# Optimization experiments

Measured on AMD Instinct MI355X. Metric: run time of the kernel, lower is better.

Reference implementation:

```python
import jax, jax.numpy as jnp
import numpy as np

BS = 320        # batch_size (per-view)
D = 128         # projection feature dim
SIGMA = 0.07    # rbf gamma = 1/sigma
C_BOX = 1.0     # box constraint on alpha
REG = 0.1       # diagonal regularizer


def setup_inputs() -> dict:
    key = jax.random.key(0)
    z = jax.random.normal(key, (2 * BS, D), dtype=jnp.float32)
    return {"z": z}


def reference(z):
    bs = z.shape[0] // 2
    nn_ = bs - 1
    dtype = z.dtype

    # L2-normalize features
    z = z / jnp.linalg.norm(z, axis=1, keepdims=True)

    gamma = 1.0 / float(SIGMA)
    K = jnp.exp(-gamma * (2.0 - 2.0 * (z[:bs] @ z.T)))        # (bs, 2bs)

    # ---- QP assembly (no-grad in original) ----
    KK = jax.lax.stop_gradient(K[:, :bs])                      # (bs, bs)
    eye = jnp.eye(bs, dtype=dtype)
    KK_d0 = KK * (1.0 - eye)
    # Delta[t,i,j] = 1 + reg*eye[i,j] + KK[i,j] - KK_d0[t,i] - KK_d0[t,j]
    Delta = (1.0 + REG * eye + KK)[None, :, :] \
            - KK_d0[:, None, :] - KK_d0[:, :, None]            # (bs, bs, bs)

    # For each t, drop row t and column t -> (bs, nn, nn)
    t_idx = jnp.arange(bs)
    j = jnp.arange(nn_)
    idx = j[None, :] + (j[None, :] >= t_idx[:, None]).astype(j.dtype)  # (bs, nn)
    DD = Delta[t_idx[:, None, None], idx[:, :, None], idx[:, None, :]]

    # Batched linear solve: DD alpha = 2*1
    rhs = 2.0 * jnp.ones((bs, nn_, 1), dtype=dtype)
    alpha_y = jnp.linalg.solve(DD, rhs)[..., 0]                # (bs, nn)
    alpha_y = jax.lax.stop_gradient(
        jnp.clip(jax.nn.relu(alpha_y), 0.0, C_BOX))
    alpha_x = alpha_y.sum(1)                                   # (bs,)

    # ---- loss terms (grad flows through K here) ----
    Ks = K[:, bs:]                                             # (bs, bs)
    # Kn = Ks^T with diagonal removed row-wise, then transposed -> (nn, bs)
    Kn = Ks.T[t_idx[:, None], idx].T

    pos_terms = jnp.diagonal(Ks)                               # (Ks * pos_mask).sum(1)
    pos_loss = (alpha_x * pos_terms).mean()
    neg_loss = (alpha_y.T * Kn).sum() / bs
    loss = neg_loss - pos_loss

    num_zero = (alpha_y == 0).sum().astype(dtype) / alpha_y.size
    sparsity = (alpha_y == C_BOX).sum().astype(dtype) / \
               ((alpha_y > 0).sum().astype(dtype) + 1e-10)

    return (loss, pos_terms.mean(), Kn.mean(), sparsity, num_zero, 0.0)
```

## Files before the change

### kernel.cpp

```cpp
#include <hip/hip_runtime.h>
#include <math.h>

#define BSZ 320
#define N2  640
#define DIM 128
#define GAM (1.0/0.07)

__device__ __forceinline__ double wave_red(double v) {
    #pragma unroll
    for (int off = 32; off > 0; off >>= 1) v += __shfl_down(v, off, 64);
    return v;
}

__launch_bounds__(640)
__global__ void k_gram(const float* __restrict__ z, double* __restrict__ E,
                       double* __restrict__ KnT, double* __restrict__ rE,
                       double* __restrict__ ssq, int* __restrict__ counter) {
    const int j  = threadIdx.x;
    const int i0 = blockIdx.x * 2;
    __shared__ float  zc[N2][36];
    __shared__ double sE[2][10], sQ[2][10];
    __shared__ double szi[2];

    if (blockIdx.x == 0 && j == 0) *counter = 0;

    double rr = 0.0;
    float  cr0 = 0.f, cr1 = 0.f;

    for (int kc = 0; kc < 4; kc++) {
        const int k0 = kc * 32;
        __syncthreads();
        #pragma unroll
        for (int it = 0; it < 8; it++) {
            int f = it * 640 + j;
            int row = f >> 3, c4 = f & 7;
            *(float4*)&zc[row][c4 * 4] = *(const float4*)(z + row * DIM + k0 + c4 * 4);
        }
        __syncthreads();
        #pragma unroll
        for (int k4 = 0; k4 < 8; k4++) {
            float4 b  = *(const float4*)&zc[j][k4 * 4];
            float4 a0 = *(const float4*)&zc[i0][k4 * 4];
            float4 a1 = *(const float4*)&zc[i0 + 1][k4 * 4];
            cr0 = fmaf(a0.x, b.x, cr0); cr1 = fmaf(a1.x, b.x, cr1);
            rr = fma((double)b.x, (double)b.x, rr);
            cr0 = fmaf(a0.y, b.y, cr0); cr1 = fmaf(a1.y, b.y, cr1);
            rr = fma((double)b.y, (double)b.y, rr);
            cr0 = fmaf(a0.z, b.z, cr0); cr1 = fmaf(a1.z, b.z, cr1);
            rr = fma((double)b.z, (double)b.z, rr);
            cr0 = fmaf(a0.w, b.w, cr0); cr1 = fmaf(a1.w, b.w, cr1);
            rr = fma((double)b.w, (double)b.w, rr);
        }
    }

    double sinv = 1.0 / sqrt(rr);
    if (j == i0)     szi[0] = sinv;
    if (j == i0 + 1) szi[1] = sinv;
    __syncthreads();
    double c0 = (double)cr0 * szi[0] * sinv;
    double c1 = (double)cr1 * szi[1] * sinv;
    double v0 = exp(-GAM * (2.0 - 2.0 * c0));
    double v1 = exp(-GAM * (2.0 - 2.0 * c1));

    double e0 = 0.0, e1 = 0.0;
    if (j < BSZ) {
        e0 = (j == i0    ) ? 0.0 : v0;
        e1 = (j == i0 + 1) ? 0.0 : v1;
        E[(i0    ) * BSZ + j] = e0;
        E[(i0 + 1) * BSZ + j] = e1;
    } else {
        KnT[(j - BSZ) * BSZ + i0    ] = v0;
        KnT[(j - BSZ) * BSZ + i0 + 1] = v1;
    }
    double q0 = e0 * e0, q1 = e1 * e1;
    e0 = wave_red(e0); q0 = wave_red(q0);
    e1 = wave_red(e1); q1 = wave_red(q1);
    int wave = j >> 6, lane = j & 63;
    if (lane == 0) { sE[0][wave] = e0; sQ[0][wave] = q0; sE[1][wave] = e1; sQ[1][wave] = q1; }
    __syncthreads();
    if (j < 2) {
        double se = 0.0, sq = 0.0;
        for (int w = 0; w < 10; w++) { se += sE[j][w]; sq += sQ[j][w]; }
        rE[i0 + j] = se; ssq[i0 + j] = sq;
    }
}

__launch_bounds__(320)
__global__ void k_cf(const double* __restrict__ E, const double* __restrict__ KnT,
                     const double* __restrict__ rE, const double* __restrict__ ssq,
                     double* __restrict__ partials, int* __restrict__ counter,
                     float* __restrict__ out) {
    const int t = blockIdx.x, tid = threadIdx.x;
    const int wave = tid >> 6, lane = tid & 63;
    __shared__ double sred[5][7];
    __shared__ double sc[8];
    __shared__ int lastflag;
    const double a = 1.0 / 1.1, c = 1.0 / 321.1;
    const double q = 1.0 - 320.0 * c;

    double rEi  = rE[tid];
    double Ereg = E[t * BSZ + tid];
    double kn   = KnT[t * BSZ + tid];
    if (tid == t) sc[6] = kn;

    {
        double s1 = wave_red(rEi);
        double s2 = wave_red(Ereg * rEi);
        if (lane == 0) { sred[wave][0] = s1; sred[wave][1] = s2; }
    }
    __syncthreads();
    if (tid == 0) {
        double S = 0, mv = 0;
        for (int w = 0; w < 5; w++) { S += sred[w][0]; mv += sred[w][1]; }
        double rEt = rE[t], ssqt = ssq[t];
        double pt  = a * q - a * a * q * (rEt - c * S);
        double b   = 320.0 * a * q - a * a * q * q * S;
        double up  = a * q * rEt - a * a * q * (mv - c * S * rEt);
        double sc1 = a * ssqt - a * c * rEt * rEt;
        double Wtt = -a * c * rEt;
        double Mtt = a * (1.0 - c) - a * a * (c * c * S - 2.0 * c * rEt);
        double s11 = 1.0 - up, s12 = -b, s21 = -sc1, s22 = 1.0 - up;
        double det = s11 * s22 - s12 * s21;
        double r1 = 2.0 * b, r2 = 2.0 * up;
        double be1 = (s22 * r1 - s12 * r2) / det;
        double be2 = (s11 * r2 - s21 * r1) / det;
        double g1  = (s22 * pt - s12 * Wtt) / det;
        double g2  = (s11 * Wtt - s21 * pt) / det;
        double ytt = 2.0 * pt + be1 * Wtt + be2 * pt;
        double dt  = Mtt + g1 * Wtt + g2 * pt;
        double rho = ytt / dt;
        sc[0] = rEt;
        sc[1] = S;
        sc[2] = 2.0 + be2 - rho * g2;
        sc[3] = be1 - rho * g1;
        sc[4] = -rho;
    }
    __syncthreads();

    {
        double rEt = sc[0], S = sc[1], cP = sc[2], cW = sc[3], cM = sc[4];
        double s_neg = 0, s_al = 0, s_kn = 0, cz = 0, c1v = 0, cpos = 0;
        if (tid != t) {
            double p_i = a * q - a * a * q * (rEi - c * S);
            double V   = a * Ereg - a * c * rEt;
            double Mi  = -a * c - a * a * (Ereg - c * (rEt + rEi) + c * c * S);
            double x = cP * p_i + cW * V + cM * Mi;
            double alpha = fmin(fmax(x, 0.0), 1.0);
            s_neg = alpha * kn; s_al = alpha; s_kn = kn;
            cz   = (x <= 0.0) ? 1.0 : 0.0;
            c1v  = (x >= 1.0) ? 1.0 : 0.0;
            cpos = (x > 0.0) ? 1.0 : 0.0;
        }
        s_neg = wave_red(s_neg); s_al = wave_red(s_al); s_kn = wave_red(s_kn);
        cz = wave_red(cz); c1v = wave_red(c1v); cpos = wave_red(cpos);
        if (lane == 0) {
            sred[wave][0] = s_neg; sred[wave][1] = s_al; sred[wave][2] = s_kn;
            sred[wave][3] = cz;    sred[wave][4] = c1v;  sred[wave][5] = cpos;
        }
    }
    __syncthreads();
    if (tid == 0) {
        double a0 = 0, a1 = 0, a2 = 0, a3 = 0, a4 = 0, a5 = 0;
        for (int w = 0; w < 5; w++) {
            a0 += sred[w][0]; a1 += sred[w][1]; a2 += sred[w][2];
            a3 += sred[w][3]; a4 += sred[w][4]; a5 += sred[w][5];
        }
        partials[t * 8 + 0] = a0;
        partials[t * 8 + 1] = a1 * sc[6];
        partials[t * 8 + 2] = a2;
        partials[t * 8 + 3] = a3;
        partials[t * 8 + 4] = a4;
        partials[t * 8 + 5] = a5;
        partials[t * 8 + 6] = sc[6];
        __threadfence();
        int ticket = atomicAdd(counter, 1);
        lastflag = (ticket == BSZ - 1) ? 1 : 0;
    }
    __syncthreads();

    if (lastflag) {
        __threadfence();
        double v0 = partials[tid * 8 + 0], v1 = partials[tid * 8 + 1];
        double v2 = partials[tid * 8 + 2], v3 = partials[tid * 8 + 3];
        double v4 = partials[tid * 8 + 4], v5 = partials[tid * 8 + 5];
        double v6 = partials[tid * 8 + 6];
        v0 = wave_red(v0); v1 = wave_red(v1); v2 = wave_red(v2);
        v3 = wave_red(v3); v4 = wave_red(v4); v5 = wave_red(v5);
        v6 = wave_red(v6);
        if (lane == 0) {
            sred[wave][0] = v0; sred[wave][1] = v1; sred[wave][2] = v2;
            sred[wave][3] = v3; sred[wave][4] = v4; sred[wave][5] = v5;
            sred[wave][6] = v6;
        }
        __syncthreads();
        if (tid == 0) {
            double b0 = 0, b1 = 0, b2 = 0, b3 = 0, b4 = 0, b5 = 0, b6 = 0;
            for (int w = 0; w < 5; w++) {
                b0 += sred[w][0]; b1 += sred[w][1]; b2 += sred[w][2];
                b3 += sred[w][3]; b4 += sred[w][4]; b5 += sred[w][5];
                b6 += sred[w][6];
            }
            out[0] = (float)((b0 - b1) / 320.0);
            out[1] = (float)(b6 / 320.0);
            out[2] = (float)(b2 / (319.0 * 320.0));
            out[3] = (float)(b4 / (b5 + 1e-10));
            out[4] = (float)(b3 / (320.0 * 319.0));
            out[5] = 0.0f;
        }
    }
}

extern "C" void kernel_launch(void* const* d_in, const int* in_sizes, int n_in,
                              void* d_out, int out_size, void* d_ws, size_t ws_size,
                              hipStream_t stream) {
    const float* z = (const float*)d_in[0];
    float* out = (float*)d_out;
    double* ws = (double*)d_ws;

    double* E        = ws;
    double* KnT      = E + 102400;
    double* rE       = KnT + 102400;
    double* ssq      = rE + 320;
    double* partials = ssq + 320;
    int* counter     = (int*)(partials + 320 * 8);

    k_gram<<<dim3(BSZ / 2), dim3(640), 0, stream>>>(z, E, KnT, rE, ssq, counter);
    k_cf  <<<dim3(BSZ), dim3(BSZ), 0, stream>>>(E, KnT, rE, ssq, partials, counter, out);
}
```

Before: 29.49 us.

## Split normalization into prep kernel and halve gram blocks across two column tiles

Adds a k_prep kernel that L2-normalizes z once into a float workspace. k_gram then runs on a 2D grid of 320-thread blocks, each covering one half of the columns, so per-block shared memory is halved and the redundant per-block double-precision norm accumulation disappears. Normalized values are now rounded to float before the dot product, which slightly changes precision, and the extra kernel launch adds overhead.

```diff
diff --git a/kernel.cpp b/kernel.cpp
--- a/kernel.cpp
+++ b/kernel.cpp
@@ -12,76 +12,81 @@
     return v;
 }
 
-__launch_bounds__(640)
-__global__ void k_gram(const float* __restrict__ z, double* __restrict__ E,
+__launch_bounds__(128)
+__global__ void k_prep(const float* __restrict__ z, float* __restrict__ zn,
+                       int* __restrict__ counter) {
+    const int row = blockIdx.x, k = threadIdx.x;
+    if (row == 0 && k == 0) *counter = 0;
+    double v = (double)z[row * DIM + k];
+    __shared__ double s2[2];
+    double w = wave_red(v * v);
+    int wave = k >> 6, lane = k & 63;
+    if (lane == 0) s2[wave] = w;
+    __syncthreads();
+    zn[row * DIM + k] = (float)(v / sqrt(s2[0] + s2[1]));
+}
+
+__launch_bounds__(320)
+__global__ void k_gram(const float* __restrict__ zn, double* __restrict__ E,
                        double* __restrict__ KnT, double* __restrict__ rE,
-                       double* __restrict__ ssq, int* __restrict__ counter) {
-    const int j  = threadIdx.x;
-    const int i0 = blockIdx.x * 2;
-    __shared__ float  zc[N2][36];
-    __shared__ double sE[2][10], sQ[2][10];
-    __shared__ double szi[2];
-
-    if (blockIdx.x == 0 && j == 0) *counter = 0;
-
-    double rr = 0.0;
-    float  cr0 = 0.f, cr1 = 0.f;
-
+                       double* __restrict__ ssq) {
+    const int tid = threadIdx.x;
+    const int i0  = blockIdx.x * 2;
+    const int jh  = blockIdx.y;
+    __shared__ float  zc[320][36];
+    __shared__ float  zi[2][128];
+    __shared__ double sE[2][5], sQ[2][5];
+
+    if (tid < 256) {
+        int r = tid >> 7, k = tid & 127;
+        zi[r][k] = zn[(i0 + r) * DIM + k];
+    }
+
+    float cr0 = 0.f, cr1 = 0.f;
     for (int kc = 0; kc < 4; kc++) {
         const int k0 = kc * 32;
         __syncthreads();
         #pragma unroll
         for (int it = 0; it < 8; it++) {
-            int f = it * 640 + j;
+            int f = it * 320 + tid;
             int row = f >> 3, c4 = f & 7;
-            *(float4*)&zc[row][c4 * 4] = *(const float4*)(z + row * DIM + k0 + c4 * 4);
+            *(float4*)&zc[row][c4 * 4] =
+                *(const float4*)(zn + (jh * 320 + row) * DIM + k0 + c4 * 4);
         }
         __syncthreads();
         #pragma unroll
         for (int k4 = 0; k4 < 8; k4++) {
-            float4 b  = *(const float4*)&zc[j][k4 * 4];
-            float4 a0 = *(const float4*)&zc[i0][k4 * 4];
-            float4 a1 = *(const float4*)&zc[i0 + 1][k4 * 4];
+            float4 b  = *(const float4*)&zc[tid][k4 * 4];
+            float4 a0 = *(const float4*)&zi[0][k0 + k4 * 4];
+            float4 a1 = *(const float4*)&zi[1][k0 + k4 * 4];
             cr0 = fmaf(a0.x, b.x, cr0); cr1 = fmaf(a1.x, b.x, cr1);
-            rr = fma((double)b.x, (double)b.x, rr);
             cr0 = fmaf(a0.y, b.y, cr0); cr1 = fmaf(a1.y, b.y, cr1);
-            rr = fma((double)b.y, (double)b.y, rr);
             cr0 = fmaf(a0.z, b.z, cr0); cr1 = fmaf(a1.z, b.z, cr1);
-            rr = fma((double)b.z, (double)b.z, rr);
             cr0 = fmaf(a0.w, b.w, cr0); cr1 = fmaf(a1.w, b.w, cr1);
-            rr = fma((double)b.w, (double)b.w, rr);
-        }
-    }
-
-    double sinv = 1.0 / sqrt(rr);
-    if (j == i0)     szi[0] = sinv;
-    if (j == i0 + 1) szi[1] = sinv;
-    __syncthreads();
-    double c0 = (double)cr0 * szi[0] * sinv;
-    double c1 = (double)cr1 * szi[1] * sinv;
-    double v0 = exp(-GAM * (2.0 - 2.0 * c0));
-    double v1 = exp(-GAM * (2.0 - 2.0 * c1));
-
-    double e0 = 0.0, e1 = 0.0;
-    if (j < BSZ) {
-        e0 = (j == i0    ) ? 0.0 : v0;
-        e1 = (j == i0 + 1) ? 0.0 : v1;
-        E[(i0    ) * BSZ + j] = e0;
-        E[(i0 + 1) * BSZ + j] = e1;
+        }
+    }
+    double v0 = exp(-GAM * (2.0 - 2.0 * (double)cr0));
+    double v1 = exp(-GAM * (2.0 - 2.0 * (double)cr1));
+    const int wave = tid >> 6, lane = tid & 63;
+    if (jh == 0) {
+        double e0 = (tid == i0    ) ? 0.0 : v0;
+        double e1 = (tid == i0 + 1) ? 0.0 : v1;
+        E[(i0    ) * BSZ + tid] = e0;
+        E[(i0 + 1) * BSZ + tid] = e1;
+        double q0 = e0 * e0, q1 = e1 * e1;
+        e0 = wave_red(e0); q0 = wave_red(q0);
+        e1 = wave_red(e1); q1 = wave_red(q1);
+        if (lane == 0) { sE[0][wave] = e0; sQ[0][wave] = q0;
+                         sE[1][wave] = e1; sQ[1][wave] = q1; }
+        __syncthreads();
+        if (tid < 2) {
+            double se = 0.0, sq = 0.0;
+            for (int w = 0; w < 5; w++) { se += sE[tid][w]; sq += sQ[tid][w]; }
+            rE[i0 + tid] = se; ssq[i0 + tid] = sq;
+        }
     } else {
-        KnT[(j - BSZ) * BSZ + i0    ] = v0;
-        KnT[(j - BSZ) * BSZ + i0 + 1] = v1;
-    }
-    double q0 = e0 * e0, q1 = e1 * e1;
-    e0 = wave_red(e0); q0 = wave_red(q0);
-    e1 = wave_red(e1); q1 = wave_red(q1);
-    int wave = j >> 6, lane = j & 63;
-    if (lane == 0) { sE[0][wave] = e0; sQ[0][wave] = q0; sE[1][wave] = e1; sQ[1][wave] = q1; }
-    __syncthreads();
-    if (j < 2) {
-        double se = 0.0, sq = 0.0;
-        for (int w = 0; w < 10; w++) { se += sE[j][w]; sq += sQ[j][w]; }
-        rE[i0 + j] = se; ssq[i0 + j] = sq;
+        KnT[tid * BSZ + i0]     = v0;
+        KnT[tid * BSZ + i0 + 1] = v1;
     }
 }
 
@@ -222,8 +227,10 @@
     double* rE       = KnT + 102400;
     double* ssq      = rE + 320;
     double* partials = ssq + 320;
-    int* counter     = (int*)(partials + 320 * 8);
-
-    k_gram<<<dim3(BSZ / 2), dim3(640), 0, stream>>>(z, E, KnT, rE, ssq, counter);
+    int*    counter  = (int*)(partials + 320 * 8);
+    float*  zn       = (float*)(counter + 16);
+
+    k_prep<<<dim3(N2), dim3(DIM), 0, stream>>>(z, zn, counter);
+    k_gram<<<dim3(BSZ / 2, 2), dim3(BSZ), 0, stream>>>(zn, E, KnT, rE, ssq);
     k_cf  <<<dim3(BSZ), dim3(BSZ), 0, stream>>>(E, KnT, rE, ssq, partials, counter, out);
 }
```

Measured after the change: 31.28 us. +6.1%, slower.
